# Kernel tuning notes

Measured on AMD Instinct MI355X. Metric: run time of the kernel, lower is better.

## Reference

```python
import math
import jax, jax.numpy as jnp
import numpy as np

B, L, U, D, H, VOCAB = 8, 512, 24, 1024, 16, 54945
T = 3 * U
CSK = 1024
BN_EPS = 1e-5


def _heads(x, H):
    b, t, dm = x.shape
    d = dm // H
    return x.reshape(b, t, H, d).transpose(0, 2, 1, 3)  # [B,H,T,d]


def _masked_attn(x, mask, edge_type, Wq, bq, Wk, bk, Wv, bv, rel_table, n_heads):
    # Faithful to MaskedSelfAttention.forward with edge_type: at query row i the
    # query/key layers have accumulated sum_{j<=i} rel_layer_j added (in-place += in torch).
    b, t, dm = x.shape
    d = dm // n_heads
    Q = _heads(x @ Wq + bq, n_heads)
    K = _heads(x @ Wk + bk, n_heads)
    V = _heads(x @ Wv + bv, n_heads)
    # rel_table[edge_type]: [B, i(rel row), p(pos), D] -> [B, i, H, p, d]
    R = rel_table[edge_type].reshape(b, t, t, n_heads, d).transpose(0, 1, 3, 2, 4)
    S = jnp.cumsum(R, axis=1)  # inclusive prefix sum over relation-row index i
    # S_diag[b,h,i,d] = S[b,i,h,i,d] : accumulated rel at query position i
    S_diag = jnp.moveaxis(jnp.diagonal(S, axis1=1, axis2=3), -1, 2)  # [B,H,T,d]
    A = Q + S_diag  # effective query rows
    # scores[b,h,i,k] = A[b,h,i] . (K[b,h,k] + S[b,i,h,k])
    scores = (jnp.einsum('bhid,bhkd->bhik', A, K)
              + jnp.einsum('bhid,bihkd->bhik', A, S)) / math.sqrt(d)
    scores = jnp.where(mask[:, None, :, :] == 0, -1e9, scores)
    probs = jax.nn.softmax(scores, axis=-1)  # dropout omitted (eval mode)
    ctx = jnp.einsum('bhik,bhkd->bhid', probs, V)
    return ctx.transpose(0, 2, 1, 3).reshape(b, t, dm)


def setup_inputs() -> dict:
    key = jax.random.key(0)
    ks = jax.random.split(key, 30)
    p = lambda k, shape: (jax.random.normal(k, shape, jnp.float32) * 0.02)
    rel_table = p(ks[8], (8, D)).at[0].set(0.0)  # padding_idx=0
    inp = {
        'hidden_states': jax.random.normal(ks[0], (B, L, D), jnp.float32),
        'emo_csk': jax.random.normal(ks[1], (B, U, CSK), jnp.float32),
        'Wq': p(ks[2], (D, D)), 'bq': jnp.zeros((D,), jnp.float32),
        'Wk': p(ks[3], (D, D)), 'bk': jnp.zeros((D,), jnp.float32),
        'Wv': p(ks[4], (D, D)), 'bv': jnp.zeros((D,), jnp.float32),
        'rel_table': rel_table,
        'fusion_W': p(ks[5], (2 * D, D)), 'fusion_b': jnp.zeros((D,), jnp.float32),
        'bn_gamma': jnp.ones((CSK,), jnp.float32), 'bn_beta': jnp.zeros((CSK,), jnp.float32),
        'bn_mean': p(ks[6], (CSK,)), 'bn_var': jnp.ones((CSK,), jnp.float32),
        'csk_W': p(ks[7], (CSK, D)), 'csk_b': jnp.zeros((D,), jnp.float32),
        'emo_W': p(ks[9], (D, 6)), 'emo_b': jnp.zeros((6,), jnp.float32),
        'str_W': p(ks[10], (D, 8)), 'str_b': jnp.zeros((8,), jnp.float32),
        'bow_W': p(ks[11], (D, VOCAB)),
        'trans_cls_index': jnp.sort(jax.random.randint(ks[12], (B, U), 2, L), axis=-1),
        'trans_graph': jax.random.randint(ks[13], (B, T, T), 0, 2, jnp.int32),
        'inter_graph': jax.random.randint(ks[14], (B, T, T), 0, 2, jnp.int32),
        'trans_edge_type': jax.random.randint(ks[15], (B, T, T), 0, 8, jnp.int32),
        'inter_edge_type': jax.random.randint(ks[16], (B, T, T), 0, 8, jnp.int32),
    }
    return inp


def reference(hidden_states, emo_csk, Wq, bq, Wk, bk, Wv, bv, rel_table,
              fusion_W, fusion_b, bn_gamma, bn_beta, bn_mean, bn_var,
              csk_W, csk_b, emo_W, emo_b, str_W, str_b, bow_W,
              trans_cls_index, trans_graph, inter_graph,
              trans_edge_type, inter_edge_type):
    b, l, dm = hidden_states.shape
    u = trans_cls_index.shape[1]
    # per-conversation CLS gather (all indices valid: text_len == U)
    cls_emb = jnp.take_along_axis(hidden_states, trans_cls_index[:, :, None], axis=1)  # [B,U,D]
    sem_cls_embs = cls_emb
    # BatchNorm1d (eval: running stats) + linear 1024->D
    csk_norm = (emo_csk - bn_mean) / jnp.sqrt(bn_var + BN_EPS) * bn_gamma + bn_beta
    csk_proj = csk_norm @ csk_W + csk_b  # [B,U,D]
    # _prepare_for_transition: [cls, cls, cls(+csk if not last)] per utterance -> T=3U
    trans_in = jnp.repeat(cls_emb, 3, axis=1)  # [B,3U,D]
    not_last = (jnp.arange(u) < u - 1).astype(csk_proj.dtype)[None, :, None]
    trans_in = trans_in.at[:, 2::3, :].add(csk_proj * not_last)
    attn = lambda x, m, e: _masked_attn(x, m, e, Wq, bq, Wk, bk, Wv, bv, rel_table, H)
    trans_out = attn(trans_in, trans_graph, trans_edge_type)
    inter_out = attn(trans_out, inter_graph, inter_edge_type)
    gate = jax.nn.sigmoid(jnp.concatenate([trans_out, inter_out], axis=-1) @ fusion_W + fusion_b)
    outputs = (1.0 - gate) * inter_out + gate * trans_out
    sem_trans = outputs[:, 0::3]
    stra_trans = outputs[:, 1::3]
    emo_trans = outputs[:, 2::3]
    last_stra_state = stra_trans[:, u - 1]
    delta = sem_trans - sem_cls_embs
    last_delta = delta[:, u - 1]
    bow_logits = delta @ bow_W
    emotion_logits = emo_trans @ emo_W + emo_b
    strategy_logits = stra_trans @ str_W + str_b
    return (last_stra_state, emo_trans, last_delta, sem_cls_embs,
            strategy_logits, emotion_logits, bow_logits)
```

## Files before the change

### kernel.cpp

```cpp
#include <hip/hip_runtime.h>
#include <math.h>

#define BB 8
#define LL 512
#define UU 24
#define DD 1024
#define HH 16
#define DH 64
#define TT 72
#define CSKN 1024
#define NVOCAB 54945

typedef __attribute__((ext_vector_type(8))) short bf16x8;
typedef __attribute__((ext_vector_type(4))) float f32x4;

__device__ inline unsigned short f2b(float x) {
    unsigned u = __float_as_uint(x);
    unsigned r = u + 0x7FFFu + ((u >> 16) & 1u);
    return (unsigned short)(r >> 16);
}
__device__ inline unsigned pack2(float lo, float hi) {
    return (unsigned)f2b(lo) | ((unsigned)f2b(hi) << 16);
}
__device__ inline void dec8(uint2 c, float* cr) {
    cr[0] = (float)( c.x        & 0xff); cr[1] = (float)((c.x >>  8) & 0xff);
    cr[2] = (float)((c.x >> 16) & 0xff); cr[3] = (float)((c.x >> 24) & 0xff);
    cr[4] = (float)( c.y        & 0xff); cr[5] = (float)((c.y >>  8) & 0xff);
    cr[6] = (float)((c.y >> 16) & 0xff); cr[7] = (float)((c.y >> 24) & 0xff);
}

__global__ __launch_bounds__(256) void k_gather_bn(const float* __restrict__ hidden,
        const int* __restrict__ idx, float* __restrict__ sem_cls, float* __restrict__ trans_in,
        const float* __restrict__ x, const float* __restrict__ g,
        const float* __restrict__ be, const float* __restrict__ mu,
        const float* __restrict__ var, float* __restrict__ y)
{
    int bid = blockIdx.x;
    if (bid < BB*UU) {
        int b = bid / UU, u = bid % UU;
        int row = idx[b*UU + u];
        const float* src = hidden + ((size_t)(b*LL + row))*DD;
        float* d0 = trans_in + ((size_t)(b*TT + 3*u))*DD;
        float* sc = sem_cls + ((size_t)(b*UU + u))*DD;
        for (int d = threadIdx.x; d < DD; d += 256) {
            float v = src[d];
            sc[d] = v;
            d0[d] = v; d0[DD + d] = v; d0[2*DD + d] = v;
        }
    } else {
        int i = (bid - BB*UU)*256 + threadIdx.x;
        int n = BB*UU*CSKN;
        if (i < n) {
            int c = i % CSKN;
            y[i] = (x[i] - mu[c]) * (1.0f/sqrtf(var[c] + 1e-5f)) * g[c] + be[c];
        }
    }
}

template<int EPI>
__global__ __launch_bounds__(256) void mm64(
        const float* __restrict__ A1, const float* __restrict__ A2, int K1,
        const float* __restrict__ Bm, const float* __restrict__ bias,
        const float* __restrict__ ep1, const float* __restrict__ ep2,
        float* __restrict__ C, int N, int K,
        const float* __restrict__ sem_cls, unsigned short* __restrict__ deltaB,
        float* __restrict__ o_emo, float* __restrict__ o_lstra,
        float* __restrict__ o_ldelta)
{
    __shared__ __align__(16) unsigned short As[2][64][72];
    __shared__ __align__(16) unsigned short Bs[2][64][72];
    int tid = threadIdx.x;
    int wave = tid >> 6, lane = tid & 63;
    int l16 = lane & 15, g = lane >> 4;
    int wm = wave & 1, wn = wave >> 1;
    int row0 = blockIdx.y * 64, col0 = blockIdx.x * 64;

    int ar = tid >> 2, akq = (tid & 3) * 16;
    int bj0 = (tid & 31) * 2, kp = tid >> 5;
    float4 a0, a1, a2, a3;
    float2 b0[4], b1[4];

    auto loadT = [&](int k0) {
        int kk = k0 + akq;
        const float* src = (kk < K1) ? A1 + (size_t)(row0+ar)*K1 + kk
                                     : A2 + (size_t)(row0+ar)*(K-K1) + (kk-K1);
        a0 = *(const float4*)src;      a1 = *(const float4*)(src+4);
        a2 = *(const float4*)(src+8);  a3 = *(const float4*)(src+12);
        #pragma unroll
        for (int s = 0; s < 4; ++s) {
            int kb = 2*(kp + 8*s);
            const float* bp = Bm + (size_t)(k0 + kb)*N + col0 + bj0;
            b0[s] = *(const float2*)bp;
            b1[s] = *(const float2*)(bp + N);
        }
    };
    auto storeT = [&](int buf) {
        unsigned* da = (unsigned*)&As[buf][ar][akq];
        da[0]=pack2(a0.x,a0.y); da[1]=pack2(a0.z,a0.w);
        da[2]=pack2(a1.x,a1.y); da[3]=pack2(a1.z,a1.w);
        da[4]=pack2(a2.x,a2.y); da[5]=pack2(a2.z,a2.w);
        da[6]=pack2(a3.x,a3.y); da[7]=pack2(a3.z,a3.w);
        #pragma unroll
        for (int s = 0; s < 4; ++s) {
            int kb = 2*(kp + 8*s);
            *(unsigned*)&Bs[buf][bj0  ][kb] = pack2(b0[s].x, b1[s].x);
            *(unsigned*)&Bs[buf][bj0+1][kb] = pack2(b0[s].y, b1[s].y);
        }
    };

    f32x4 acc[2][2] = {};
    loadT(0); storeT(0);
    __syncthreads();
    int nt = K / 64;
    for (int t = 0; t < nt; ++t) {
        int cur = t & 1;
        if (t + 1 < nt) loadT((t+1)*64);
        #pragma unroll
        for (int kk = 0; kk < 2; ++kk) {
            bf16x8 af[2], bfr[2];
            #pragma unroll
            for (int mf = 0; mf < 2; ++mf) af[mf] = *(const bf16x8*)&As[cur][wm*32 + mf*16 + l16][kk*32 + g*8];
            #pragma unroll
            for (int nf = 0; nf < 2; ++nf) bfr[nf] = *(const bf16x8*)&Bs[cur][wn*32 + nf*16 + l16][kk*32 + g*8];
            #pragma unroll
            for (int mf = 0; mf < 2; ++mf)
                #pragma unroll
                for (int nf = 0; nf < 2; ++nf)
                    acc[mf][nf] = __builtin_amdgcn_mfma_f32_16x16x32_bf16(af[mf], bfr[nf], acc[mf][nf], 0, 0, 0);
        }
        if (t + 1 < nt) storeT(cur ^ 1);
        __syncthreads();
    }
    #pragma unroll
    for (int mf = 0; mf < 2; ++mf)
        #pragma unroll
        for (int nf = 0; nf < 2; ++nf) {
            int cc = col0 + wn*32 + nf*16 + l16;
            float bv = bias[cc];
            #pragma unroll
            for (int r = 0; r < 4; ++r) {
                int rr = row0 + wm*32 + mf*16 + g*4 + r;
                float v = acc[mf][nf][r] + bv;
                if (EPI == 4) {
                    int bq = rr / UU, uq = rr % UU;
                    if (uq < UU-1) {
                        float* dst = &C[((size_t)(bq*TT + 3*uq + 2))*DD + cc];
                        *dst += v;
                    }
                } else {
                    float gg = 1.0f/(1.0f + __expf(-v));
                    float tv = ep1[(size_t)rr*N + cc];
                    float iv = ep2[(size_t)rr*N + cc];
                    float bl = gg*tv + (1.0f - gg)*iv;
                    C[(size_t)rr*N + cc] = bl;
                    int b = rr / TT, tt = rr % TT;
                    int m3 = tt % 3, u = tt / 3;
                    if (m3 == 0) {
                        float dl = bl - sem_cls[((size_t)(b*UU + u))*DD + cc];
                        deltaB[((size_t)(b*UU + u))*DD + cc] = f2b(dl);
                        if (u == UU-1) o_ldelta[b*DD + cc] = dl;
                    } else if (m3 == 1) {
                        if (u == UU-1) o_lstra[b*DD + cc] = bl;
                    } else {
                        o_emo[((size_t)(b*UU + u))*DD + cc] = bl;
                    }
                }
            }
        }
}

__global__ __launch_bounds__(256) void mm_qkv(
        const float* __restrict__ x,
        const float* __restrict__ W0, const float* __restrict__ W1, const float* __restrict__ W2,
        const float* __restrict__ v0, const float* __restrict__ v1, const float* __restrict__ v2,
        float* __restrict__ C0, float* __restrict__ C1, float* __restrict__ C2)
{
    __shared__ __align__(16) unsigned short As[2][64][72];
    __shared__ __align__(16) unsigned short Bs[2][64][72];
    int which = blockIdx.x >> 4;
    int col0 = (blockIdx.x & 15) * 64;
    int row0 = blockIdx.y * 64;
    const float* W  = (which == 0) ? W0 : (which == 1) ? W1 : W2;
    const float* bb = (which == 0) ? v0 : (which == 1) ? v1 : v2;
    float*       C  = (which == 0) ? C0 : (which == 1) ? C1 : C2;
    int tid = threadIdx.x;
    int wave = tid >> 6, lane = tid & 63;
    int l16 = lane & 15, g = lane >> 4;
    int wm = wave & 1, wn = wave >> 1;

    int ar = tid >> 2, akq = (tid & 3) * 16;
    int bj0 = (tid & 31) * 2, kp = tid >> 5;
    float4 a0, a1, a2, a3;
    float2 b0[4], b1[4];

    auto loadT = [&](int k0) {
        const float* src = x + (size_t)(row0+ar)*DD + k0 + akq;
        a0 = *(const float4*)src;      a1 = *(const float4*)(src+4);
        a2 = *(const float4*)(src+8);  a3 = *(const float4*)(src+12);
        #pragma unroll
        for (int s = 0; s < 4; ++s) {
            int kb = 2*(kp + 8*s);
            const float* bp = W + (size_t)(k0 + kb)*DD + col0 + bj0;
            b0[s] = *(const float2*)bp;
            b1[s] = *(const float2*)(bp + DD);
        }
    };
    auto storeT = [&](int buf) {
        unsigned* da = (unsigned*)&As[buf][ar][akq];
        da[0]=pack2(a0.x,a0.y); da[1]=pack2(a0.z,a0.w);
        da[2]=pack2(a1.x,a1.y); da[3]=pack2(a1.z,a1.w);
        da[4]=pack2(a2.x,a2.y); da[5]=pack2(a2.z,a2.w);
        da[6]=pack2(a3.x,a3.y); da[7]=pack2(a3.z,a3.w);
        #pragma unroll
        for (int s = 0; s < 4; ++s) {
            int kb = 2*(kp + 8*s);
            *(unsigned*)&Bs[buf][bj0  ][kb] = pack2(b0[s].x, b1[s].x);
            *(unsigned*)&Bs[buf][bj0+1][kb] = pack2(b0[s].y, b1[s].y);
        }
    };

    f32x4 acc[2][2] = {};
    loadT(0); storeT(0);
    __syncthreads();
    for (int t = 0; t < 16; ++t) {
        int cur = t & 1;
        if (t < 15) loadT((t+1)*64);
        #pragma unroll
        for (int kk = 0; kk < 2; ++kk) {
            bf16x8 af[2], bfr[2];
            #pragma unroll
            for (int mf = 0; mf < 2; ++mf) af[mf] = *(const bf16x8*)&As[cur][wm*32 + mf*16 + l16][kk*32 + g*8];
            #pragma unroll
            for (int nf = 0; nf < 2; ++nf) bfr[nf] = *(const bf16x8*)&Bs[cur][wn*32 + nf*16 + l16][kk*32 + g*8];
            #pragma unroll
            for (int mf = 0; mf < 2; ++mf)
                #pragma unroll
                for (int nf = 0; nf < 2; ++nf)
                    acc[mf][nf] = __builtin_amdgcn_mfma_f32_16x16x32_bf16(af[mf], bfr[nf], acc[mf][nf], 0, 0, 0);
        }
        if (t < 15) storeT(cur ^ 1);
        __syncthreads();
    }
    #pragma unroll
    for (int mf = 0; mf < 2; ++mf)
        #pragma unroll
        for (int nf = 0; nf < 2; ++nf) {
            int cc = col0 + wn*32 + nf*16 + l16;
            float bv = bb[cc];
            #pragma unroll
            for (int r = 0; r < 4; ++r) {
                int rr = row0 + wm*32 + mf*16 + g*4 + r;
                C[(size_t)rr*DD + cc] = acc[mf][nf][r] + bv;
            }
        }
}

__global__ __launch_bounds__(256, 1) void mm_bow(
        const unsigned short* __restrict__ Ab, const float* __restrict__ Bm,
        float* __restrict__ C)
{
    __shared__ __align__(16) unsigned short A_lds[192][136];
    const int N = NVOCAB;
    int tid = threadIdx.x;
    int lane = tid & 63, wave = tid >> 6;
    int l16 = lane & 15, g = lane >> 4;
    int col = blockIdx.x * 64 + wave * 16 + l16;
    int colc = (col < N) ? col : (N - 1);
    const float* bbase = Bm + (size_t)(g * 8) * N + colc;

    int4 areg0, areg1, areg2, areg3, areg4, areg5, areg6, areg7, areg8, areg9, areg10, areg11;
#define AIDX(i) int r##i = ((i)*256 + tid) >> 4, c##i = (((i)*256 + tid) & 15) * 8
    AIDX(0); AIDX(1); AIDX(2); AIDX(3); AIDX(4); AIDX(5);
    AIDX(6); AIDX(7); AIDX(8); AIDX(9); AIDX(10); AIDX(11);
#undef AIDX
#define LOADA(s) {                                                             \
        const unsigned short* ab = Ab + (s)*128;                               \
        areg0  = *(const int4*)(ab + (size_t)r0*DD  + c0);                     \
        areg1  = *(const int4*)(ab + (size_t)r1*DD  + c1);                     \
        areg2  = *(const int4*)(ab + (size_t)r2*DD  + c2);                     \
        areg3  = *(const int4*)(ab + (size_t)r3*DD  + c3);                     \
        areg4  = *(const int4*)(ab + (size_t)r4*DD  + c4);                     \
        areg5  = *(const int4*)(ab + (size_t)r5*DD  + c5);                     \
        areg6  = *(const int4*)(ab + (size_t)r6*DD  + c6);                     \
        areg7  = *(const int4*)(ab + (size_t)r7*DD  + c7);                     \
        areg8  = *(const int4*)(ab + (size_t)r8*DD  + c8);                     \
        areg9  = *(const int4*)(ab + (size_t)r9*DD  + c9);                     \
        areg10 = *(const int4*)(ab + (size_t)r10*DD + c10);                    \
        areg11 = *(const int4*)(ab + (size_t)r11*DD + c11);                    \
    }
#define WRITEA() {                                                             \
        *(int4*)&A_lds[r0][c0]   = areg0;  *(int4*)&A_lds[r1][c1]   = areg1;   \
        *(int4*)&A_lds[r2][c2]   = areg2;  *(int4*)&A_lds[r3][c3]   = areg3;   \
        *(int4*)&A_lds[r4][c4]   = areg4;  *(int4*)&A_lds[r5][c5]   = areg5;   \
        *(int4*)&A_lds[r6][c6]   = areg6;  *(int4*)&A_lds[r7][c7]   = areg7;   \
        *(int4*)&A_lds[r8][c8]   = areg8;  *(int4*)&A_lds[r9][c9]   = areg9;   \
        *(int4*)&A_lds[r10][c10] = areg10; *(int4*)&A_lds[r11][c11] = areg11;  \
    }

    f32x4 acc[12] = {};
    float bs[4][8];

#define LOADB(dst, t_) { const float* bp = bbase + (size_t)(t_) * 32 * N;      \
        _Pragma("unroll") for (int j = 0; j < 8; ++j) dst[j] = bp[(size_t)j * N]; }
#define PACKB(fr, sv) { _Pragma("unroll") for (int j = 0; j < 8; ++j)          \
        ((unsigned short*)&fr)[j] = f2b(sv[j]); }

    LOADA(0); WRITEA();
    #pragma unroll
    for (int p = 0; p < 4; ++p) LOADB(bs[p], p);
    __syncthreads();

    for (int s = 0; s < 8; ++s) {
        if (s < 7) LOADA(s + 1);
        #pragma unroll
        for (int p = 0; p < 4; ++p) {
            int P = s*4 + p;
            bf16x8 fr;
            PACKB(fr, bs[p]);
            if (P + 4 < 32) LOADB(bs[p], P + 4);
            #pragma unroll
            for (int mf = 0; mf < 12; ++mf) {
                bf16x8 af = *(const bf16x8*)&A_lds[mf*16 + l16][p*32 + g*8];
                acc[mf] = __builtin_amdgcn_mfma_f32_16x16x32_bf16(af, fr, acc[mf], 0, 0, 0);
            }
        }
        if (s < 7) {
            __syncthreads();
            WRITEA();
            __syncthreads();
        }
    }
#undef LOADA
#undef WRITEA
#undef LOADB
#undef PACKB
    if (col < N) {
        #pragma unroll
        for (int mf = 0; mf < 12; ++mf)
            #pragma unroll
            for (int r = 0; r < 4; ++r)
                C[(size_t)(mf * 16 + g * 4 + r) * N + col] = acc[mf][r];
    }
}

__global__ __launch_bounds__(512) void k_attn(const float* __restrict__ Qb,
        const float* __restrict__ Kg, const float* __restrict__ Vg,
        const int* __restrict__ et, const float* __restrict__ rel,
        const int* __restrict__ mask, float* __restrict__ out)
{
    int bid = blockIdx.x;
    int is = bid & 1;
    int h  = (bid >> 1) & (HH-1);
    int b  = bid >> 5;
    int lo = is * (TT/2);
    __shared__ float K_sh[DH][TT+1];
    __shared__ float V_sh[TT][DH];
    __shared__ uint2 cnt_sh[TT/2][TT];
    __shared__ __align__(16) unsigned char un_raw[6400];
    float (*rel_sh)[DH] = (float(*)[DH])un_raw;
    float (*a_row)[DH]  = (float(*)[DH])(un_raw + 2048);
    float (*p_row)[TT]  = (float(*)[TT])(un_raw + 4096);
    unsigned char* e_sh = un_raw;
    int tid = threadIdx.x;
    int lane = tid & 63, w = tid >> 6;

    for (int idx = tid; idx < TT*16; idx += 512) {
        int r = idx >> 4, q4 = (idx & 15) * 4;
        size_t goff = ((size_t)(b*TT + r))*DD + h*DH + q4;
        float4 kv = *(const float4*)&Kg[goff];
        K_sh[q4  ][r] = kv.x; K_sh[q4+1][r] = kv.y;
        K_sh[q4+2][r] = kv.z; K_sh[q4+3][r] = kv.w;
        float4 vv = *(const float4*)&Vg[goff];
        *(float4*)&V_sh[r][q4] = vv;
    }
    for (int idx = tid; idx < (TT*TT)/4; idx += 512) {
        int4 v = ((const int4*)(et + (size_t)b*TT*TT))[idx];
        unsigned pk = (unsigned)v.x | ((unsigned)v.y << 8) | ((unsigned)v.z << 16) | ((unsigned)v.w << 24);
        *(unsigned*)&e_sh[idx*4] = pk;
    }
    __syncthreads();
    if (tid < TT) {
        unsigned lo32 = 0, hi32 = 0;
        int iend = lo + TT/2;
        for (int i = 0; i < iend; ++i) {
            int r = e_sh[i*TT + tid];
            if (r < 4) lo32 += 1u << (8*r); else hi32 += 1u << (8*(r-4));
            if (i >= lo) cnt_sh[i - lo][tid] = make_uint2(lo32, hi32);
        }
    }
    __syncthreads();
    if (tid < 128) {
        int r = tid >> 4, q4 = (tid & 15) * 4;
        *(float4*)&rel_sh[r][q4] = *(const float4*)&rel[r*DD + h*DH + q4];
    }
    __syncthreads();

    auto processRow = [&](float q, int ii) {
        int i = lo + ii;
        size_t rowoff = (size_t)(b*TT + i);
        float crd[8]; dec8(cnt_sh[ii][i], crd);
        float a = q;
        #pragma unroll
        for (int r = 0; r < 8; ++r) a += crd[r]*rel_sh[r][lane];
        a_row[w][lane] = a;
        float arr[8];
        #pragma unroll
        for (int r = 0; r < 8; ++r) {
            float pr = a * rel_sh[r][lane];
            #pragma unroll
            for (int off = 32; off; off >>= 1) pr += __shfl_xor(pr, off);
            arr[r] = pr;
        }
        float s1;
        {
            int t = lane;
            float s = 0.0f;
            #pragma unroll
            for (int d0 = 0; d0 < DH; d0 += 4) {
                float4 av = *(const float4*)&a_row[w][d0];
                s += av.x*K_sh[d0][t] + av.y*K_sh[d0+1][t]
                   + av.z*K_sh[d0+2][t] + av.w*K_sh[d0+3][t];
            }
            float cr2[8]; dec8(cnt_sh[ii][t], cr2);
            float s2v = cr2[0]*arr[0] + cr2[1]*arr[1] + cr2[2]*arr[2] + cr2[3]*arr[3]
                      + cr2[4]*arr[4] + cr2[5]*arr[5] + cr2[6]*arr[6] + cr2[7]*arr[7];
            int m = mask[rowoff*TT + t];
            s1 = (m == 0) ? -1e9f : (s + s2v)*0.125f;
        }
        float s2 = -1e30f;
        if (lane < TT - DH) {
            int t = DH + lane;
            float s = 0.0f;
            #pragma unroll
            for (int d0 = 0; d0 < DH; d0 += 4) {
                float4 av = *(const float4*)&a_row[w][d0];
                s += av.x*K_sh[d0][t] + av.y*K_sh[d0+1][t]
                   + av.z*K_sh[d0+2][t] + av.w*K_sh[d0+3][t];
            }
            float cr2[8]; dec8(cnt_sh[ii][t], cr2);
            float s2v = cr2[0]*arr[0] + cr2[1]*arr[1] + cr2[2]*arr[2] + cr2[3]*arr[3]
                      + cr2[4]*arr[4] + cr2[5]*arr[5] + cr2[6]*arr[6] + cr2[7]*arr[7];
            int m = mask[rowoff*TT + t];
            s2 = (m == 0) ? -1e9f : (s + s2v)*0.125f;
        }
        float mx = fmaxf(s1, s2);
        #pragma unroll
        for (int off = 32; off; off >>= 1) mx = fmaxf(mx, __shfl_xor(mx, off));
        float e1 = __expf(s1 - mx);
        float e2 = (lane < TT - DH) ? __expf(s2 - mx) : 0.0f;
        float sm = e1 + e2;
        #pragma unroll
        for (int off = 32; off; off >>= 1) sm += __shfl_xor(sm, off);
        float inv = 1.0f / sm;
        p_row[w][lane] = e1 * inv;
        if (lane < TT - DH) p_row[w][DH + lane] = e2 * inv;
        float o = 0.0f;
        #pragma unroll 8
        for (int t = 0; t < TT; ++t) o += p_row[w][t] * V_sh[t][lane];
        out[rowoff*DD + h*DH + lane] = o;
    };

    float qv0, qv1, qv2, qv3, qv4 = 0.0f;
    {
        size_t base = ((size_t)(b*TT + lo + w))*DD + h*DH + lane;
        qv0 = Qb[base];
        qv1 = Qb[base + (size_t)8*DD];
        qv2 = Qb[base + (size_t)16*DD];
        qv3 = Qb[base + (size_t)24*DD];
        if (w < 4) qv4 = Qb[base + (size_t)32*DD];
    }
    processRow(qv0, w);
    processRow(qv1, w + 8);
    processRow(qv2, w + 16);
    processRow(qv3, w + 24);
    if (w < 4) processRow(qv4, w + 32);
}

__global__ __launch_bounds__(256) void k_logits(const float* __restrict__ outs,
        const float* __restrict__ strW, const float* __restrict__ strB,
        const float* __restrict__ emoW, const float* __restrict__ emoB,
        float* __restrict__ o_str, float* __restrict__ o_emo_log)
{
    __shared__ float part[14][16];
    int bid = blockIdx.x; int b = bid / UU, u = bid % UU;
    const float* st = outs + ((size_t)(b*TT + 3*u + 1))*DD;
    const float* em = st + DD;
    int t = threadIdx.x;
    if (t < 224) {
        int o = t >> 4, c = t & 15;
        float s = 0.0f;
        if (o < 8) {
            for (int d = c*64; d < c*64 + 64; ++d) s += st[d]*strW[d*8 + o];
        } else {
            int j = o - 8;
            for (int d = c*64; d < c*64 + 64; ++d) s += em[d]*emoW[d*6 + j];
        }
        part[o][c] = s;
    }
    __syncthreads();
    if (t < 14) {
        float s = 0.0f;
        #pragma unroll
        for (int c2 = 0; c2 < 16; ++c2) s += part[t][c2];
        if (t < 8) o_str[(b*UU + u)*8 + t] = s + strB[t];
        else       o_emo_log[(b*UU + u)*6 + (t-8)] = s + emoB[t-8];
    }
}

extern "C" void kernel_launch(void* const* d_in, const int* in_sizes, int n_in,
                              void* d_out, int out_size, void* d_ws, size_t ws_size,
                              hipStream_t stream)
{
    const float* hidden  = (const float*)d_in[0];
    const float* emo_csk = (const float*)d_in[1];
    const float* Wq  = (const float*)d_in[2];
    const float* bq  = (const float*)d_in[3];
    const float* Wk  = (const float*)d_in[4];
    const float* bk  = (const float*)d_in[5];
    const float* Wv  = (const float*)d_in[6];
    const float* bv  = (const float*)d_in[7];
    const float* rel = (const float*)d_in[8];
    const float* fusW = (const float*)d_in[9];
    const float* fusB = (const float*)d_in[10];
    const float* bng = (const float*)d_in[11];
    const float* bnb = (const float*)d_in[12];
    const float* bnm = (const float*)d_in[13];
    const float* bnv = (const float*)d_in[14];
    const float* cskW = (const float*)d_in[15];
    const float* cskB = (const float*)d_in[16];
    const float* emoW = (const float*)d_in[17];
    const float* emoB = (const float*)d_in[18];
    const float* strW = (const float*)d_in[19];
    const float* strB = (const float*)d_in[20];
    const float* bowW = (const float*)d_in[21];
    const int* clsIdx = (const int*)d_in[22];
    const int* tGraph = (const int*)d_in[23];
    const int* iGraph = (const int*)d_in[24];
    const int* tEdge  = (const int*)d_in[25];
    const int* iEdge  = (const int*)d_in[26];

    float* out = (float*)d_out;
    float* o_last_stra  = out;
    float* o_emo_trans  = out + 8192;
    float* o_last_delta = out + 204800;
    float* o_sem_cls    = out + 212992;
    float* o_str_log    = out + 409600;
    float* o_emo_log    = out + 411136;
    float* o_bow        = out + 412288;

    float* ws = (float*)d_ws;
    const int SZ_BTD = BB*TT*DD;
    const int SZ_BUD = BB*UU*DD;
    float* trans_in  = ws;
    float* Qb        = trans_in + SZ_BTD;
    float* Kb        = Qb + SZ_BTD;
    float* Vb        = Kb + SZ_BTD;
    float* trans_out = Vb + SZ_BTD;
    float* inter_out = trans_out + SZ_BTD;
    float* outsB     = inter_out + SZ_BTD;
    float* csk_norm  = outsB + SZ_BTD;
    unsigned short* deltaB = (unsigned short*)(csk_norm + SZ_BUD);

    k_gather_bn<<<dim3(BB*UU + (BB*UU*CSKN+255)/256), dim3(256), 0, stream>>>(
            hidden, clsIdx, o_sem_cls, trans_in, emo_csk, bng, bnb, bnm, bnv, csk_norm);
    mm64<4><<<dim3(16, 3), dim3(256), 0, stream>>>(csk_norm, nullptr, CSKN, cskW, cskB,
            nullptr, nullptr, trans_in, DD, CSKN, nullptr, nullptr, nullptr, nullptr, nullptr);

    auto attention = [&](const float* x, const int* graph, const int* edge, float* ctx_out) {
        mm_qkv<<<dim3(48, (BB*TT)/64), dim3(256), 0, stream>>>(x, Wq, Wk, Wv, bq, bk, bv, Qb, Kb, Vb);
        k_attn<<<dim3(BB*HH*2), dim3(512), 0, stream>>>(Qb, Kb, Vb, edge, rel, graph, ctx_out);
    };
    attention(trans_in, tGraph, tEdge, trans_out);
    attention(trans_out, iGraph, iEdge, inter_out);

    mm64<5><<<dim3(16, (BB*TT)/64), dim3(256), 0, stream>>>(trans_out, inter_out, DD, fusW, fusB,
            trans_out, inter_out, outsB, DD, 2*DD,
            o_sem_cls, deltaB, o_emo_trans, o_last_stra, o_last_delta);

    k_logits<<<dim3(BB*UU), dim3(256), 0, stream>>>(outsB, strW, strB, emoW, emoB,
            o_str_log, o_emo_log);

    mm_bow<<<dim3((NVOCAB+63)/64), dim3(256), 0, stream>>>(deltaB, bowW, o_bow);
}
```

Before: 263.9 us.

## Split bow GEMM rows across waves to drop block barriers and raise occupancy

mm_bow now gives each block 16 vocab columns and has each of the 4 waves compute a separate 48-row slice, with a private LDS region per wave. Because no wave reads another wave's LDS data, all __syncthreads calls are removed. The launch_bounds minimum-blocks hint is dropped and the grid grows fourfold, aiming for more resident waves to hide latency on the large weight stream. In exchange, the 4 waves of a block each load the same B columns, and the full A matrix is re-read by four times as many blocks, which raises L2 traffic.

```diff
diff --git a/kernel.cpp b/kernel.cpp
--- a/kernel.cpp
+++ b/kernel.cpp
@@ -255,49 +255,49 @@
         }
 }
 
-__global__ __launch_bounds__(256, 1) void mm_bow(
+__global__ __launch_bounds__(256) void mm_bow(
         const unsigned short* __restrict__ Ab, const float* __restrict__ Bm,
         float* __restrict__ C)
 {
-    __shared__ __align__(16) unsigned short A_lds[192][136];
+    __shared__ __align__(16) unsigned short A_lds[4][48][136];
     const int N = NVOCAB;
     int tid = threadIdx.x;
-    int lane = tid & 63, wave = tid >> 6;
+    int lane = tid & 63, w = tid >> 6;
     int l16 = lane & 15, g = lane >> 4;
-    int col = blockIdx.x * 64 + wave * 16 + l16;
+    int col = blockIdx.x * 16 + l16;
     int colc = (col < N) ? col : (N - 1);
     const float* bbase = Bm + (size_t)(g * 8) * N + colc;
 
-    int4 areg0, areg1, areg2, areg3, areg4, areg5, areg6, areg7, areg8, areg9, areg10, areg11;
-#define AIDX(i) int r##i = ((i)*256 + tid) >> 4, c##i = (((i)*256 + tid) & 15) * 8
+    int4 ar0, ar1, ar2, ar3, ar4, ar5, ar6, ar7, ar8, ar9, ar10, ar11;
+#define AIDX(i) int rr##i = ((i)*64 + lane) >> 4, ck##i = (((i)*64 + lane) & 15) * 8
     AIDX(0); AIDX(1); AIDX(2); AIDX(3); AIDX(4); AIDX(5);
     AIDX(6); AIDX(7); AIDX(8); AIDX(9); AIDX(10); AIDX(11);
 #undef AIDX
-#define LOADA(s) {                                                             \
-        const unsigned short* ab = Ab + (s)*128;                               \
-        areg0  = *(const int4*)(ab + (size_t)r0*DD  + c0);                     \
-        areg1  = *(const int4*)(ab + (size_t)r1*DD  + c1);                     \
-        areg2  = *(const int4*)(ab + (size_t)r2*DD  + c2);                     \
-        areg3  = *(const int4*)(ab + (size_t)r3*DD  + c3);                     \
-        areg4  = *(const int4*)(ab + (size_t)r4*DD  + c4);                     \
-        areg5  = *(const int4*)(ab + (size_t)r5*DD  + c5);                     \
-        areg6  = *(const int4*)(ab + (size_t)r6*DD  + c6);                     \
-        areg7  = *(const int4*)(ab + (size_t)r7*DD  + c7);                     \
-        areg8  = *(const int4*)(ab + (size_t)r8*DD  + c8);                     \
-        areg9  = *(const int4*)(ab + (size_t)r9*DD  + c9);                     \
-        areg10 = *(const int4*)(ab + (size_t)r10*DD + c10);                    \
-        areg11 = *(const int4*)(ab + (size_t)r11*DD + c11);                    \
+    const unsigned short* abase = Ab + (size_t)(w * 48) * DD;
+#define LOADA(s) { const unsigned short* ab = abase + (s) * 128;               \
+        ar0  = *(const int4*)(ab + (size_t)rr0*DD  + ck0);                     \
+        ar1  = *(const int4*)(ab + (size_t)rr1*DD  + ck1);                     \
+        ar2  = *(const int4*)(ab + (size_t)rr2*DD  + ck2);                     \
+        ar3  = *(const int4*)(ab + (size_t)rr3*DD  + ck3);                     \
+        ar4  = *(const int4*)(ab + (size_t)rr4*DD  + ck4);                     \
+        ar5  = *(const int4*)(ab + (size_t)rr5*DD  + ck5);                     \
+        ar6  = *(const int4*)(ab + (size_t)rr6*DD  + ck6);                     \
+        ar7  = *(const int4*)(ab + (size_t)rr7*DD  + ck7);                     \
+        ar8  = *(const int4*)(ab + (size_t)rr8*DD  + ck8);                     \
+        ar9  = *(const int4*)(ab + (size_t)rr9*DD  + ck9);                     \
+        ar10 = *(const int4*)(ab + (size_t)rr10*DD + ck10);                    \
+        ar11 = *(const int4*)(ab + (size_t)rr11*DD + ck11);                    \
     }
 #define WRITEA() {                                                             \
-        *(int4*)&A_lds[r0][c0]   = areg0;  *(int4*)&A_lds[r1][c1]   = areg1;   \
-        *(int4*)&A_lds[r2][c2]   = areg2;  *(int4*)&A_lds[r3][c3]   = areg3;   \
-        *(int4*)&A_lds[r4][c4]   = areg4;  *(int4*)&A_lds[r5][c5]   = areg5;   \
-        *(int4*)&A_lds[r6][c6]   = areg6;  *(int4*)&A_lds[r7][c7]   = areg7;   \
-        *(int4*)&A_lds[r8][c8]   = areg8;  *(int4*)&A_lds[r9][c9]   = areg9;   \
-        *(int4*)&A_lds[r10][c10] = areg10; *(int4*)&A_lds[r11][c11] = areg11;  \
-    }
-
-    f32x4 acc[12] = {};
+        *(int4*)&A_lds[w][rr0][ck0]   = ar0;  *(int4*)&A_lds[w][rr1][ck1]   = ar1; \
+        *(int4*)&A_lds[w][rr2][ck2]   = ar2;  *(int4*)&A_lds[w][rr3][ck3]   = ar3; \
+        *(int4*)&A_lds[w][rr4][ck4]   = ar4;  *(int4*)&A_lds[w][rr5][ck5]   = ar5; \
+        *(int4*)&A_lds[w][rr6][ck6]   = ar6;  *(int4*)&A_lds[w][rr7][ck7]   = ar7; \
+        *(int4*)&A_lds[w][rr8][ck8]   = ar8;  *(int4*)&A_lds[w][rr9][ck9]   = ar9; \
+        *(int4*)&A_lds[w][rr10][ck10] = ar10; *(int4*)&A_lds[w][rr11][ck11] = ar11; \
+    }
+
+    f32x4 acc[3] = {};
     float bs[4][8];
 
 #define LOADB(dst, t_) { const float* bp = bbase + (size_t)(t_) * 32 * N;      \
@@ -308,7 +308,6 @@
     LOADA(0); WRITEA();
     #pragma unroll
     for (int p = 0; p < 4; ++p) LOADB(bs[p], p);
-    __syncthreads();
 
     for (int s = 0; s < 8; ++s) {
         if (s < 7) LOADA(s + 1);
@@ -319,16 +318,12 @@
             PACKB(fr, bs[p]);
             if (P + 4 < 32) LOADB(bs[p], P + 4);
             #pragma unroll
-            for (int mf = 0; mf < 12; ++mf) {
-                bf16x8 af = *(const bf16x8*)&A_lds[mf*16 + l16][p*32 + g*8];
+            for (int mf = 0; mf < 3; ++mf) {
+                bf16x8 af = *(const bf16x8*)&A_lds[w][mf*16 + l16][p*32 + g*8];
                 acc[mf] = __builtin_amdgcn_mfma_f32_16x16x32_bf16(af, fr, acc[mf], 0, 0, 0);
             }
         }
-        if (s < 7) {
-            __syncthreads();
-            WRITEA();
-            __syncthreads();
-        }
+        if (s < 7) WRITEA();
     }
 #undef LOADA
 #undef WRITEA
@@ -336,10 +331,10 @@
 #undef PACKB
     if (col < N) {
         #pragma unroll
-        for (int mf = 0; mf < 12; ++mf)
+        for (int mf = 0; mf < 3; ++mf)
             #pragma unroll
             for (int r = 0; r < 4; ++r)
-                C[(size_t)(mf * 16 + g * 4 + r) * N + col] = acc[mf][r];
+                C[(size_t)(w*48 + mf*16 + g*4 + r) * N + col] = acc[mf][r];
     }
 }
 
@@ -580,5 +575,5 @@
     k_logits<<<dim3(BB*UU), dim3(256), 0, stream>>>(outsB, strW, strB, emoW, emoB,
             o_str_log, o_emo_log);
 
-    mm_bow<<<dim3((NVOCAB+63)/64), dim3(256), 0, stream>>>(deltaB, bowW, o_bow);
-}
+    mm_bow<<<dim3((NVOCAB+15)/16), dim3(256), 0, stream>>>(deltaB, bowW, o_bow);
+}
```

New measurement: 374.9 us. 1.42x slower.

## Retile bow GEMM to 256-column blocks with 2x4 wave grid

Applied to the files above, without the earlier changes.

The vocabulary projection kernel now uses 512-thread blocks covering 256 output columns. Each wave computes a 96-row by 64-column tile, so A fragments read from LDS are reused across four B column fragments instead of one. The A tile in LDS is shared by four times as many columns, cutting redundant A loads from global memory. In exchange the grid has far fewer blocks (about 215 versus about 859), B prefetch depth drops from four k-slices to two, and per-thread register pressure rises.

```diff
diff --git a/kernel.cpp b/kernel.cpp
--- a/kernel.cpp
+++ b/kernel.cpp
@@ -255,7 +255,7 @@
         }
 }
 
-__global__ __launch_bounds__(256, 1) void mm_bow(
+__global__ __launch_bounds__(512) void mm_bow(
         const unsigned short* __restrict__ Ab, const float* __restrict__ Bm,
         float* __restrict__ C)
 {
@@ -264,50 +264,50 @@
     int tid = threadIdx.x;
     int lane = tid & 63, wave = tid >> 6;
     int l16 = lane & 15, g = lane >> 4;
-    int col = blockIdx.x * 64 + wave * 16 + l16;
-    int colc = (col < N) ? col : (N - 1);
-    const float* bbase = Bm + (size_t)(g * 8) * N + colc;
-
-    int4 areg0, areg1, areg2, areg3, areg4, areg5, areg6, areg7, areg8, areg9, areg10, areg11;
-#define AIDX(i) int r##i = ((i)*256 + tid) >> 4, c##i = (((i)*256 + tid) & 15) * 8
+    int wr = wave & 1, wc = wave >> 1;
+    int colq = blockIdx.x * 256 + wc * 64;
+
+    const float* bbase0;
+    const float* bbase1;
+    const float* bbase2;
+    const float* bbase3;
+    {
+        int c0_ = colq + 0*16 + l16;  bbase0 = Bm + (size_t)(g*8)*N + ((c0_ < N) ? c0_ : (N-1));
+        int c1_ = colq + 1*16 + l16;  bbase1 = Bm + (size_t)(g*8)*N + ((c1_ < N) ? c1_ : (N-1));
+        int c2_ = colq + 2*16 + l16;  bbase2 = Bm + (size_t)(g*8)*N + ((c2_ < N) ? c2_ : (N-1));
+        int c3_ = colq + 3*16 + l16;  bbase3 = Bm + (size_t)(g*8)*N + ((c3_ < N) ? c3_ : (N-1));
+    }
+
+    int4 aA, aB, aC, aD, aE, aF;
+#define AIDX(i) int r##i = ((i)*512 + tid) >> 4, c##i = (((i)*512 + tid) & 15) * 8
     AIDX(0); AIDX(1); AIDX(2); AIDX(3); AIDX(4); AIDX(5);
-    AIDX(6); AIDX(7); AIDX(8); AIDX(9); AIDX(10); AIDX(11);
 #undef AIDX
-#define LOADA(s) {                                                             \
-        const unsigned short* ab = Ab + (s)*128;                               \
-        areg0  = *(const int4*)(ab + (size_t)r0*DD  + c0);                     \
-        areg1  = *(const int4*)(ab + (size_t)r1*DD  + c1);                     \
-        areg2  = *(const int4*)(ab + (size_t)r2*DD  + c2);                     \
-        areg3  = *(const int4*)(ab + (size_t)r3*DD  + c3);                     \
-        areg4  = *(const int4*)(ab + (size_t)r4*DD  + c4);                     \
-        areg5  = *(const int4*)(ab + (size_t)r5*DD  + c5);                     \
-        areg6  = *(const int4*)(ab + (size_t)r6*DD  + c6);                     \
-        areg7  = *(const int4*)(ab + (size_t)r7*DD  + c7);                     \
-        areg8  = *(const int4*)(ab + (size_t)r8*DD  + c8);                     \
-        areg9  = *(const int4*)(ab + (size_t)r9*DD  + c9);                     \
-        areg10 = *(const int4*)(ab + (size_t)r10*DD + c10);                    \
-        areg11 = *(const int4*)(ab + (size_t)r11*DD + c11);                    \
+#define LOADA(s) { const unsigned short* ab = Ab + (s)*128;                    \
+        aA = *(const int4*)(ab + (size_t)r0*DD + c0);                          \
+        aB = *(const int4*)(ab + (size_t)r1*DD + c1);                          \
+        aC = *(const int4*)(ab + (size_t)r2*DD + c2);                          \
+        aD = *(const int4*)(ab + (size_t)r3*DD + c3);                          \
+        aE = *(const int4*)(ab + (size_t)r4*DD + c4);                          \
+        aF = *(const int4*)(ab + (size_t)r5*DD + c5);                          \
     }
 #define WRITEA() {                                                             \
-        *(int4*)&A_lds[r0][c0]   = areg0;  *(int4*)&A_lds[r1][c1]   = areg1;   \
-        *(int4*)&A_lds[r2][c2]   = areg2;  *(int4*)&A_lds[r3][c3]   = areg3;   \
-        *(int4*)&A_lds[r4][c4]   = areg4;  *(int4*)&A_lds[r5][c5]   = areg5;   \
-        *(int4*)&A_lds[r6][c6]   = areg6;  *(int4*)&A_lds[r7][c7]   = areg7;   \
-        *(int4*)&A_lds[r8][c8]   = areg8;  *(int4*)&A_lds[r9][c9]   = areg9;   \
-        *(int4*)&A_lds[r10][c10] = areg10; *(int4*)&A_lds[r11][c11] = areg11;  \
-    }
-
-    f32x4 acc[12] = {};
-    float bs[4][8];
-
-#define LOADB(dst, t_) { const float* bp = bbase + (size_t)(t_) * 32 * N;      \
-        _Pragma("unroll") for (int j = 0; j < 8; ++j) dst[j] = bp[(size_t)j * N]; }
+        *(int4*)&A_lds[r0][c0] = aA;  *(int4*)&A_lds[r1][c1] = aB;             \
+        *(int4*)&A_lds[r2][c2] = aC;  *(int4*)&A_lds[r3][c3] = aD;             \
+        *(int4*)&A_lds[r4][c4] = aE;  *(int4*)&A_lds[r5][c5] = aF;             \
+    }
+
+    f32x4 acc[6][4] = {};
+    float bs[2][4][8];
+
+#define LOADB1(slot, nf, base, t_) { const float* bp = (base) + (size_t)(t_) * 32 * N; \
+        _Pragma("unroll") for (int j = 0; j < 8; ++j) bs[slot][nf][j] = bp[(size_t)j * N]; }
+#define LOADB(slot, t_) { LOADB1(slot, 0, bbase0, t_); LOADB1(slot, 1, bbase1, t_); \
+                          LOADB1(slot, 2, bbase2, t_); LOADB1(slot, 3, bbase3, t_); }
 #define PACKB(fr, sv) { _Pragma("unroll") for (int j = 0; j < 8; ++j)          \
         ((unsigned short*)&fr)[j] = f2b(sv[j]); }
 
     LOADA(0); WRITEA();
-    #pragma unroll
-    for (int p = 0; p < 4; ++p) LOADB(bs[p], p);
+    LOADB(0, 0); LOADB(1, 1);
     __syncthreads();
 
     for (int s = 0; s < 8; ++s) {
@@ -315,13 +315,27 @@
         #pragma unroll
         for (int p = 0; p < 4; ++p) {
             int P = s*4 + p;
-            bf16x8 fr;
-            PACKB(fr, bs[p]);
-            if (P + 4 < 32) LOADB(bs[p], P + 4);
-            #pragma unroll
-            for (int mf = 0; mf < 12; ++mf) {
-                bf16x8 af = *(const bf16x8*)&A_lds[mf*16 + l16][p*32 + g*8];
-                acc[mf] = __builtin_amdgcn_mfma_f32_16x16x32_bf16(af, fr, acc[mf], 0, 0, 0);
+            bf16x8 af0 = *(const bf16x8*)&A_lds[wr*96 + 0*16 + l16][p*32 + g*8];
+            bf16x8 af1 = *(const bf16x8*)&A_lds[wr*96 + 1*16 + l16][p*32 + g*8];
+            bf16x8 af2 = *(const bf16x8*)&A_lds[wr*96 + 2*16 + l16][p*32 + g*8];
+            bf16x8 af3 = *(const bf16x8*)&A_lds[wr*96 + 3*16 + l16][p*32 + g*8];
+            bf16x8 af4 = *(const bf16x8*)&A_lds[wr*96 + 4*16 + l16][p*32 + g*8];
+            bf16x8 af5 = *(const bf16x8*)&A_lds[wr*96 + 5*16 + l16][p*32 + g*8];
+            #pragma unroll
+            for (int nf = 0; nf < 4; ++nf) {
+                bf16x8 fr;
+                PACKB(fr, bs[p & 1][nf]);
+                if (P + 2 < 32) {
+                    const float* base = (nf == 0) ? bbase0 : (nf == 1) ? bbase1
+                                       : (nf == 2) ? bbase2 : bbase3;
+                    LOADB1(p & 1, nf, base, P + 2);
+                }
+                acc[0][nf] = __builtin_amdgcn_mfma_f32_16x16x32_bf16(af0, fr, acc[0][nf], 0, 0, 0);
+                acc[1][nf] = __builtin_amdgcn_mfma_f32_16x16x32_bf16(af1, fr, acc[1][nf], 0, 0, 0);
+                acc[2][nf] = __builtin_amdgcn_mfma_f32_16x16x32_bf16(af2, fr, acc[2][nf], 0, 0, 0);
+                acc[3][nf] = __builtin_amdgcn_mfma_f32_16x16x32_bf16(af3, fr, acc[3][nf], 0, 0, 0);
+                acc[4][nf] = __builtin_amdgcn_mfma_f32_16x16x32_bf16(af4, fr, acc[4][nf], 0, 0, 0);
+                acc[5][nf] = __builtin_amdgcn_mfma_f32_16x16x32_bf16(af5, fr, acc[5][nf], 0, 0, 0);
             }
         }
         if (s < 7) {
@@ -333,13 +347,18 @@
 #undef LOADA
 #undef WRITEA
 #undef LOADB
+#undef LOADB1
 #undef PACKB
-    if (col < N) {
-        #pragma unroll
-        for (int mf = 0; mf < 12; ++mf)
-            #pragma unroll
-            for (int r = 0; r < 4; ++r)
-                C[(size_t)(mf * 16 + g * 4 + r) * N + col] = acc[mf][r];
+    #pragma unroll
+    for (int nf = 0; nf < 4; ++nf) {
+        int cc = colq + nf*16 + l16;
+        if (cc < N) {
+            #pragma unroll
+            for (int mf = 0; mf < 6; ++mf)
+                #pragma unroll
+                for (int r = 0; r < 4; ++r)
+                    C[(size_t)(wr*96 + mf*16 + g*4 + r) * N + cc] = acc[mf][nf][r];
+        }
     }
 }
 
@@ -580,5 +599,5 @@
     k_logits<<<dim3(BB*UU), dim3(256), 0, stream>>>(outsB, strW, strB, emoW, emoB,
             o_str_log, o_emo_log);
 
-    mm_bow<<<dim3((NVOCAB+63)/64), dim3(256), 0, stream>>>(deltaB, bowW, o_bow);
-}
+    mm_bow<<<dim3((NVOCAB+255)/256), dim3(512), 0, stream>>>(deltaB, bowW, o_bow);
+}
```

New measurement: 324.1 us. 22.8% more time.
